# Kernel tuning notes

Measured on AMD Instinct MI355X. Metric: run time of the kernel, lower is better.

Reference implementation:

```python
import jax, jax.numpy as jnp
import numpy as np

N_NODE = 100_000
N_EDGE = 2_000_000
IN_DIM = 64
OUT_DIM = 64
ATTN_DIM = 32
N_REL = 200   # rela_embed has 2*N_REL+1 = 401 rows
N_ENT = 50_000
BATCH = 8


def setup_inputs() -> dict:
    key = jax.random.key(0)
    ks = jax.random.split(key, 16)
    # edges columns: 0=r_idx (query index in batch), 2=rel, 4=sub, 5=obj; cols 1,3 unused
    r_idx = jax.random.randint(ks[0], (N_EDGE,), 0, BATCH, dtype=jnp.int32)
    rel = jax.random.randint(ks[1], (N_EDGE,), 0, 2 * N_REL + 1, dtype=jnp.int32)
    sub = jax.random.randint(ks[2], (N_EDGE,), 0, N_NODE, dtype=jnp.int32)
    obj = jax.random.randint(ks[3], (N_EDGE,), 0, N_NODE, dtype=jnp.int32)
    pad = jnp.zeros((N_EDGE,), jnp.int32)
    edges = jnp.stack([r_idx, pad, rel, pad, sub, obj], axis=1)
    nodes = jnp.stack(
        [jax.random.randint(ks[4], (N_NODE,), 0, BATCH, dtype=jnp.int32),
         jax.random.randint(ks[5], (N_NODE,), 0, N_ENT, dtype=jnp.int32)], axis=1)
    s = 0.05
    return {
        "q_sub": jax.random.randint(ks[6], (BATCH,), 0, N_ENT, dtype=jnp.int32),
        "q_rel": jax.random.randint(ks[7], (BATCH,), 0, 2 * N_REL + 1, dtype=jnp.int32),
        "hidden": jax.random.normal(ks[8], (N_NODE, IN_DIM), jnp.float32),
        "edges": edges,
        "nodes": nodes,
        "old_nodes_new_idx": jnp.arange(N_NODE // 2, dtype=jnp.int32),
        "batchsize": BATCH,
        "rela_embed": jax.random.normal(ks[9], (2 * N_REL + 1, IN_DIM), jnp.float32) * s,
        "Ws": jax.random.normal(ks[10], (ATTN_DIM, IN_DIM), jnp.float32) * s,
        "Wr": jax.random.normal(ks[11], (ATTN_DIM, IN_DIM), jnp.float32) * s,
        "Wqr": jax.random.normal(ks[12], (ATTN_DIM, IN_DIM), jnp.float32) * s,
        "bqr": jax.random.normal(ks[13], (ATTN_DIM,), jnp.float32) * s,
        "w_alpha_w": jax.random.normal(ks[14], (1, ATTN_DIM), jnp.float32) * s,
        "w_alpha_b": jnp.zeros((1,), jnp.float32),
        "Wh": jax.random.normal(ks[15], (OUT_DIM, IN_DIM), jnp.float32) * s,
    }


def reference(q_sub, q_rel, hidden, edges, nodes, old_nodes_new_idx, batchsize,
              rela_embed, Ws, Wr, Wqr, bqr, w_alpha_w, w_alpha_b, Wh):
    sub = edges[:, 4]
    rel = edges[:, 2]
    obj = edges[:, 5]
    r_idx = edges[:, 0]
    n_node = hidden.shape[0]

    hs = hidden[sub]                      # [E, in_dim] gather
    hr = rela_embed[rel]                  # [E, in_dim] gather
    h_qr = rela_embed[q_rel][r_idx]       # [E, in_dim] gather of per-query rel embed

    # attention: sigmoid(w_alpha(relu(Ws hs + Wr hr + Wqr h_qr + bqr)))
    attn = jax.nn.relu(hs @ Ws.T + hr @ Wr.T + h_qr @ Wqr.T + bqr)  # [E, attn_dim]
    alpha = jax.nn.sigmoid(attn @ w_alpha_w.T + w_alpha_b)           # [E, 1]

    message = alpha * (hs + hr)           # [E, in_dim]
    message_agg = jax.ops.segment_sum(message, obj, num_segments=n_node)  # [n_node, in_dim]
    hidden_new = message_agg @ Wh.T       # act is identity (default)
    return hidden_new
```

## Files before the change

### kernel.cpp

```cpp
#include <hip/hip_runtime.h>
#include <hip/hip_bf16.h>
#include <hip/hip_fp16.h>


typedef __attribute__((ext_vector_type(8))) short bf16x8;
typedef __attribute__((ext_vector_type(4))) float f32x4;
typedef __attribute__((ext_vector_type(2))) float f32x2;

__device__ inline unsigned short f2bf(float x) {
    unsigned u = __float_as_uint(x);
    u += 0x7FFF + ((u >> 16) & 1);
    return (unsigned short)(u >> 16);
}
__device__ inline float bf2f(unsigned short b) {
    return __uint_as_float(((unsigned)b) << 16);
}
__device__ inline __half2 u2h2(unsigned u) {
    return __builtin_bit_cast(__half2, u);
}

__device__ inline bf16x8 pack8(float4 a, float4 b) {
    bf16x8 r;
    r[0] = (short)f2bf(a.x); r[1] = (short)f2bf(a.y);
    r[2] = (short)f2bf(a.z); r[3] = (short)f2bf(a.w);
    r[4] = (short)f2bf(b.x); r[5] = (short)f2bf(b.y);
    r[6] = (short)f2bf(b.z); r[7] = (short)f2bf(b.w);
    return r;
}

template<int NT, bool F16>
__global__ void proj_mfma2_kernel(const float* __restrict__ X1, int n1,
                                  const float* __restrict__ X2, int n2,
                                  const float* __restrict__ W,
                                  unsigned short* __restrict__ out1,
                                  unsigned short* __restrict__ out2) {
    int nb1 = (n1 + 63) / 64;
    const float* X; unsigned short* out; int nrows, mblk;
    if ((int)blockIdx.x < nb1) { X = X1; out = out1; nrows = n1; mblk = blockIdx.x; }
    else                        { X = X2; out = out2; nrows = n2; mblk = blockIdx.x - nb1; }

    int lane = threadIdx.x & 63;
    int wv   = threadIdx.x >> 6;
    int m0   = (mblk * 4 + wv) * 16;
    if (m0 >= nrows) return;
    int lr = lane & 15;
    int lk = lane >> 4;

    bf16x8 bfr[NT][2];
#pragma unroll
    for (int nt = 0; nt < NT; ++nt)
#pragma unroll
        for (int ks = 0; ks < 2; ++ks) {
            const float* wp = W + (size_t)(nt * 16 + lr) * 64 + ks * 32 + lk * 8;
            float4 w0 = *(const float4*)wp;
            float4 w1 = *(const float4*)(wp + 4);
            bfr[nt][ks] = pack8(w0, w1);
        }

    int row = m0 + lr;
    if (row >= nrows) row = nrows - 1;
    const float* xp = X + (size_t)row * 64 + lk * 8;
    float4 x0 = *(const float4*)xp;
    float4 x1 = *(const float4*)(xp + 4);
    float4 x2 = *(const float4*)(xp + 32);
    float4 x3 = *(const float4*)(xp + 36);
    bf16x8 a0 = pack8(x0, x1);
    bf16x8 a1 = pack8(x2, x3);

    f32x4 acc[NT];
#pragma unroll
    for (int nt = 0; nt < NT; ++nt) {
        acc[nt] = (f32x4){0.f, 0.f, 0.f, 0.f};
        acc[nt] = __builtin_amdgcn_mfma_f32_16x16x32_bf16(a0, bfr[nt][0], acc[nt], 0, 0, 0);
        acc[nt] = __builtin_amdgcn_mfma_f32_16x16x32_bf16(a1, bfr[nt][1], acc[nt], 0, 0, 0);
    }

#pragma unroll
    for (int nt = 0; nt < NT; ++nt)
#pragma unroll
        for (int r = 0; r < 4; ++r) {
            int ro = m0 + lk * 4 + r;
            if (ro < nrows) {
                unsigned short bits;
                if (F16) {
                    __half h = __float2half(acc[nt][r]);
                    bits = __builtin_bit_cast(unsigned short, h);
                } else {
                    bits = f2bf(acc[nt][r]);
                }
                out[(size_t)ro * (NT * 16) + nt * 16 + lr] = bits;
            }
        }
}

__global__ void qproj_bf16_kernel(const int* __restrict__ q_rel, const float* __restrict__ rela,
                                  const float* __restrict__ Wqr, const float* __restrict__ bqr,
                                  unsigned* __restrict__ Qb, int batch) {
    int tid = threadIdx.x;
    int b = tid >> 5, k = tid & 31;
    if (b >= batch) return;
    int qr = q_rel[b];
    const float* x = rela + (size_t)qr * 64;
    const float* w = Wqr + (size_t)k * 64;
    float acc = bqr[k];
    for (int d = 0; d < 64; ++d) acc += w[d] * x[d];
    float other = __shfl_xor(acc, 1, 64);
    if ((k & 1) == 0) {
        unsigned lo = f2bf(acc), hi = f2bf(other);
        Qb[b * 16 + (k >> 1)] = lo | (hi << 16);
    }
}

__global__ void pack_hist_kernel(const int4* __restrict__ edges4, int2* __restrict__ pk2,
                                 int* __restrict__ hmat, int n_edge, int NB) {
    __shared__ int hist[256];
    int tid = threadIdx.x, blk = blockIdx.x;
    hist[tid] = 0;
    __syncthreads();
    int unit0 = blk * 2048;
#pragma unroll
    for (int k = 0; k < 8; ++k) {
        int u = unit0 + k * 256 + tid;
        int base = u * 4;
        if (base >= n_edge) break;
        if (base + 4 <= n_edge) {
            const int4* p = edges4 + (size_t)u * 6;
            int4 v0 = p[0], v1 = p[1], v2 = p[2], v3 = p[3], v4 = p[4], v5 = p[5];
            atomicAdd(&hist[v1.y >> 9], 1);
            atomicAdd(&hist[v2.w >> 9], 1);
            atomicAdd(&hist[v4.y >> 9], 1);
            atomicAdd(&hist[v5.w >> 9], 1);
            int4 o0, o1;
            o0.x = v1.x | (v0.z << 17); o0.y = v1.y | (v0.x << 17);
            o0.z = v2.z | (v2.x << 17); o0.w = v2.w | (v1.z << 17);
            o1.x = v4.x | (v3.z << 17); o1.y = v4.y | (v3.x << 17);
            o1.z = v5.z | (v5.x << 17); o1.w = v5.w | (v4.z << 17);
            int4* q = (int4*)pk2 + (size_t)u * 2;
            q[0] = o0;
            q[1] = o1;
        } else {
            const int* ei = (const int*)edges4;
            for (int e = base; e < n_edge; ++e) {
                const int* ep = ei + (size_t)e * 6;
                int ridx = ep[0], rel = ep[2], sub = ep[4], obj = ep[5];
                atomicAdd(&hist[obj >> 9], 1);
                pk2[e] = make_int2(sub | (rel << 17), obj | (ridx << 17));
            }
        }
    }
    __syncthreads();
    hmat[tid * NB + blk] = hist[tid];
}

#define SCAN_CHUNK 1024

__global__ void scan_partial_kernel(const int* __restrict__ counts, int* __restrict__ bsum,
                                    int N) {
    __shared__ int s[256];
    int base = blockIdx.x * SCAN_CHUNK;
    int tid = threadIdx.x;
    int sum = 0;
#pragma unroll
    for (int k = 0; k < 4; ++k) {
        int idx = base + k * 256 + tid;
        if (idx < N) sum += counts[idx];
    }
    s[tid] = sum;
    __syncthreads();
    for (int off = 128; off > 0; off >>= 1) {
        if (tid < off) s[tid] += s[tid + off];
        __syncthreads();
    }
    if (tid == 0) bsum[blockIdx.x] = s[0];
}

__global__ void scan_bsum_kernel(int* __restrict__ bsum, int* __restrict__ offs, int B, int N) {
    __shared__ int s[1024];
    int tid = threadIdx.x;
    int v = (tid < B) ? bsum[tid] : 0;
    s[tid] = v;
    __syncthreads();
    for (int off = 1; off < 1024; off <<= 1) {
        int t = (tid >= off) ? s[tid - off] : 0;
        __syncthreads();
        s[tid] += t;
        __syncthreads();
    }
    if (tid < B) bsum[tid] = s[tid] - v;
    if (tid == 0) offs[N] = s[1023];
}

__global__ void scan_final_kernel(const int* __restrict__ counts, const int* __restrict__ bsum,
                                  int* __restrict__ offs, int N) {
    __shared__ int s[256];
    int base = blockIdx.x * SCAN_CHUNK;
    int tid = threadIdx.x;
    int v[4];
    int sum = 0;
#pragma unroll
    for (int k = 0; k < 4; ++k) {
        int idx = base + tid * 4 + k;
        v[k] = (idx < N) ? counts[idx] : 0;
        sum += v[k];
    }
    s[tid] = sum;
    __syncthreads();
    for (int off = 1; off < 256; off <<= 1) {
        int t = (tid >= off) ? s[tid - off] : 0;
        __syncthreads();
        s[tid] += t;
        __syncthreads();
    }
    int run = bsum[blockIdx.x] + s[tid] - sum;
#pragma unroll
    for (int k = 0; k < 4; ++k) {
        int idx = base + tid * 4 + k;
        if (idx < N) offs[idx] = run;
        run += v[k];
    }
}

__global__ void scatter1_kernel(const int2* __restrict__ pk2, const int* __restrict__ hscan,
                                int2* __restrict__ outrec, int n_edge, int NB) {
    __shared__ int cur[256];
    int tid = threadIdx.x, blk = blockIdx.x;
    cur[tid] = hscan[tid * NB + blk];
    __syncthreads();
    int unit0 = blk * 2048;
#pragma unroll
    for (int k = 0; k < 8; ++k) {
        int u = unit0 + k * 256 + tid;
        int base = u * 4;
        if (base >= n_edge) break;
        if (base + 4 <= n_edge) {
            const int4* q = (const int4*)pk2 + (size_t)u * 2;
            int4 a = q[0], b = q[1];
            int p0 = atomicAdd(&cur[(a.y >> 9) & 0xFF], 1);
            int p1 = atomicAdd(&cur[(a.w >> 9) & 0xFF], 1);
            int p2 = atomicAdd(&cur[(b.y >> 9) & 0xFF], 1);
            int p3 = atomicAdd(&cur[(b.w >> 9) & 0xFF], 1);
            outrec[p0] = make_int2(a.x, a.y);
            outrec[p1] = make_int2(a.z, a.w);
            outrec[p2] = make_int2(b.x, b.y);
            outrec[p3] = make_int2(b.z, b.w);
        } else {
            for (int e = base; e < n_edge; ++e) {
                int2 r = pk2[e];
                int p = atomicAdd(&cur[(r.y >> 9) & 0xFF], 1);
                outrec[p] = r;
            }
        }
    }
}

#define BS_CAP 12288
__global__ __launch_bounds__(512) void bucket_sort_kernel(const int2* __restrict__ in,
                                                          const int* __restrict__ hscan,
                                                          int2* __restrict__ out,
                                                          int* __restrict__ offs,
                                                          int NB, int n_node) {
    __shared__ int hist[512];
    __shared__ int sbase[512];
    __shared__ int cur[512];
    __shared__ int2 st[BS_CAP];
    int b = blockIdx.x, tid = threadIdx.x;
    int start = hscan[b * NB];
    int end   = hscan[(b + 1) * NB];
    int size  = end - start;
    hist[tid] = 0;
    __syncthreads();
    bool inlds = (size <= BS_CAP);
    if (inlds) {
        for (int i = tid; i < size; i += 512) {
            int2 v = in[start + i];
            st[i] = v;
            atomicAdd(&hist[v.y & 511], 1);
        }
    } else {
        for (int i = tid; i < size; i += 512) {
            int2 v = in[start + i];
            atomicAdd(&hist[v.y & 511], 1);
        }
    }
    __syncthreads();
    int h = hist[tid];
    sbase[tid] = h;
    __syncthreads();
    for (int off = 1; off < 512; off <<= 1) {
        int t = (tid >= off) ? sbase[tid - off] : 0;
        __syncthreads();
        sbase[tid] += t;
        __syncthreads();
    }
    int ebase = sbase[tid] - h;
    cur[tid] = ebase;
    int obj = (b << 9) | tid;
    if (obj <= n_node) offs[obj] = start + ebase;
    __syncthreads();
    if (inlds) {
        for (int i = tid; i < size; i += 512) {
            int2 r = st[i];
            int p = atomicAdd(&cur[r.y & 511], 1);
            out[start + p] = r;
        }
    } else {
        for (int i = tid; i < size; i += 512) {
            int2 r = in[start + i];
            int p = atomicAdd(&cur[r.y & 511], 1);
            out[start + p] = r;
        }
    }
}

__device__ inline float edot(unsigned sv, unsigned rv, unsigned qv, float2 w) {
    float a0 = fmaxf(bf2f((unsigned short)sv) + bf2f((unsigned short)rv)
                     + bf2f((unsigned short)qv), 0.f);
    float a1 = fmaxf(bf2f((unsigned short)(sv >> 16)) + bf2f((unsigned short)(rv >> 16))
                     + bf2f((unsigned short)(qv >> 16)), 0.f);
    return a0 * w.x + a1 * w.y;
}

__global__ void alpha_kernel(const int2* __restrict__ pk2,
                             const unsigned* __restrict__ Sb,
                             const unsigned* __restrict__ Rb,
                             const unsigned* __restrict__ Qb,
                             const float2* __restrict__ w2,
                             const float* __restrict__ w_alpha_b,
                             float2* __restrict__ rec,
                             int n_edge) {
    int tid = threadIdx.x;
    int lane = tid & 15;
    int e0 = (blockIdx.x * 16 + (tid >> 4)) * 4;
    if (e0 >= n_edge) return;
    int eN = n_edge - 1;
    int2 h0 = pk2[e0];
    int2 h1 = pk2[min(e0 + 1, eN)];
    int2 h2 = pk2[min(e0 + 2, eN)];
    int2 h3 = pk2[min(e0 + 3, eN)];
    float2 w = w2[lane];
    unsigned sv0 = Sb[(size_t)(h0.x & 0x1FFFF) * 16 + lane];
    unsigned sv1 = Sb[(size_t)(h1.x & 0x1FFFF) * 16 + lane];
    unsigned sv2 = Sb[(size_t)(h2.x & 0x1FFFF) * 16 + lane];
    unsigned sv3 = Sb[(size_t)(h3.x & 0x1FFFF) * 16 + lane];
    unsigned rv0 = Rb[(size_t)(h0.x >> 17) * 16 + lane];
    unsigned rv1 = Rb[(size_t)(h1.x >> 17) * 16 + lane];
    unsigned rv2 = Rb[(size_t)(h2.x >> 17) * 16 + lane];
    unsigned rv3 = Rb[(size_t)(h3.x >> 17) * 16 + lane];
    unsigned qv0 = Qb[((h0.y >> 17) & 7) * 16 + lane];
    unsigned qv1 = Qb[((h1.y >> 17) & 7) * 16 + lane];
    unsigned qv2 = Qb[((h2.y >> 17) & 7) * 16 + lane];
    unsigned qv3 = Qb[((h3.y >> 17) & 7) * 16 + lane];
    float p0 = edot(sv0, rv0, qv0, w);
    float p1 = edot(sv1, rv1, qv1, w);
    float p2 = edot(sv2, rv2, qv2, w);
    float p3 = edot(sv3, rv3, qv3, w);
#pragma unroll
    for (int off = 8; off > 0; off >>= 1) {
        p0 += __shfl_xor(p0, off, 16);
        p1 += __shfl_xor(p1, off, 16);
        p2 += __shfl_xor(p2, off, 16);
        p3 += __shfl_xor(p3, off, 16);
    }
    if (lane < 4 && e0 + lane < n_edge) {
        float p = p0; int2 h = h0;
        if (lane == 1) { p = p1; h = h1; }
        if (lane == 2) { p = p2; h = h2; }
        if (lane == 3) { p = p3; h = h3; }
        float alpha = 1.f / (1.f + __expf(-(p + w_alpha_b[0])));
        float2 out;
        out.x = alpha;
        out.y = __int_as_float(h.x);
        rec[e0 + lane] = out;
    }
}

__global__ void reduce_kernel(const float2* __restrict__ rec, const int* __restrict__ offs,
                              const uint2* __restrict__ Hw2,
                              const uint2* __restrict__ Rw2,
                              float4* __restrict__ out4, int n_node) {
    int lane = threadIdx.x & 63;
    int node = blockIdx.x * 4 + (threadIdx.x >> 6);
    if (node >= n_node) return;
    int g = lane >> 4;
    int t = lane & 15;
    int start = offs[node], end = offs[node + 1];
    __half2 acc0 = __float2half2_rn(0.f);
    __half2 acc1 = __float2half2_rn(0.f);

    for (int i = start; i < end; i += 64) {
        int m = end - i;
        if (m > 64) m = 64;
        float a = 0.f;
        int pk = 0;
        if (lane < m) {
            f32x2 r = __builtin_nontemporal_load((const f32x2*)&rec[i + lane]);
            a = r.x;
            pk = __float_as_int(r.y);
        }
        int nj = (m + 3) >> 2;

        __half2 A0, A1, A2, A3;
        uint2 H0, H1, H2, H3, R0, R1, R2, R3;

#define RD_ISSUE(S, J) do {                                                   \
        int src_ = 4 * (J) + g;                                               \
        bool ok_ = (src_ < m);                                                \
        int s_ = ok_ ? src_ : 0;                                              \
        float a_ = __shfl(a, s_, 64);                                         \
        int p_ = __shfl(pk, s_, 64);                                          \
        A##S = __float2half2_rn(ok_ ? a_ : 0.f);                              \
        int sub_ = p_ & 0x1FFFF, rel_ = p_ >> 17;                             \
        H##S = Hw2[(size_t)sub_ * 16 + t];                                    \
        R##S = Rw2[(size_t)rel_ * 16 + t];                                    \
    } while (0)

#define RD_CONSUME(S) do {                                                    \
        acc0 = __hfma2(A##S, __hadd2(u2h2(H##S.x), u2h2(R##S.x)), acc0);      \
        acc1 = __hfma2(A##S, __hadd2(u2h2(H##S.y), u2h2(R##S.y)), acc1);      \
    } while (0)

        RD_ISSUE(0, 0);
        RD_ISSUE(1, 1);
        RD_ISSUE(2, 2);
        RD_ISSUE(3, 3);
        for (int j = 0; j < nj; j += 4) {
            RD_CONSUME(0); RD_ISSUE(0, j + 4);
            RD_CONSUME(1); RD_ISSUE(1, j + 5);
            RD_CONSUME(2); RD_ISSUE(2, j + 6);
            RD_CONSUME(3); RD_ISSUE(3, j + 7);
        }
#undef RD_ISSUE
#undef RD_CONSUME
    }
    float2 f0 = __half22float2(acc0);
    float2 f1 = __half22float2(acc1);
    f32x4 acc = (f32x4){f0.x, f0.y, f1.x, f1.y};
#pragma unroll
    for (int off = 16; off <= 32; off <<= 1) {
        acc.x += __shfl_xor(acc.x, off, 64);
        acc.y += __shfl_xor(acc.y, off, 64);
        acc.z += __shfl_xor(acc.z, off, 64);
        acc.w += __shfl_xor(acc.w, off, 64);
    }
    if (g == 0)
        __builtin_nontemporal_store(acc, (f32x4*)&out4[(size_t)node * 16 + t]);
}

extern "C" void kernel_launch(void* const* d_in, const int* in_sizes, int n_in,
                              void* d_out, int out_size, void* d_ws, size_t ws_size,
                              hipStream_t stream) {
    const int*   q_rel     = (const int*)d_in[1];
    const float* hidden    = (const float*)d_in[2];
    const int*   edges     = (const int*)d_in[3];
    const float* rela      = (const float*)d_in[7];
    const float* Ws        = (const float*)d_in[8];
    const float* Wr        = (const float*)d_in[9];
    const float* Wqr       = (const float*)d_in[10];
    const float* bqr       = (const float*)d_in[11];
    const float* w_alpha_w = (const float*)d_in[12];
    const float* w_alpha_b = (const float*)d_in[13];
    const float* Wh        = (const float*)d_in[14];

    int n_node = in_sizes[2] / 64;
    int n_edge = in_sizes[3] / 6;
    int n_rel  = in_sizes[7] / 64;
    int batch  = in_sizes[1];

    int NB = (n_edge + 8191) / 8192;
    int N2 = NB * 256;
    int n_sblk2 = (N2 + SCAN_CHUNK - 1) / SCAN_CHUNK;

    unsigned* Sb   = (unsigned*)d_ws;
    unsigned* Rb   = Sb + (size_t)n_node * 16;
    unsigned* Qb   = Rb + (size_t)n_rel * 16;
    int*   offs    = (int*)(Qb + (size_t)batch * 16);
    int*   bsum    = offs + n_node + 1;
    int*   hmat    = bsum + 1024;
    int*   hscan   = hmat + N2;
    size_t rec_off = (size_t)(hscan + N2 + 1 - (int*)d_ws);
    rec_off = (rec_off + 3) & ~(size_t)3;
    float2* rec    = (float2*)((int*)d_ws + rec_off);
    int2*  pk2     = (int2*)(rec + n_edge);
    unsigned short* Hw = (unsigned short*)pk2;
    unsigned short* Rw = Hw + (size_t)n_node * 64;

    {
        int nb = (n_node + 63) / 64 + (n_rel + 63) / 64;
        proj_mfma2_kernel<2, false><<<nb, 256, 0, stream>>>(
            hidden, n_node, rela, n_rel, Ws, (unsigned short*)Sb, (unsigned short*)Rb);
    }
    qproj_bf16_kernel<<<1, 256, 0, stream>>>(q_rel, rela, Wqr, bqr, Qb, batch);

    pack_hist_kernel<<<NB, 256, 0, stream>>>((const int4*)edges, pk2, hmat, n_edge, NB);

    scan_partial_kernel<<<n_sblk2, 256, 0, stream>>>(hmat, bsum, N2);
    scan_bsum_kernel<<<1, 1024, 0, stream>>>(bsum, hscan, n_sblk2, N2);
    scan_final_kernel<<<n_sblk2, 256, 0, stream>>>(hmat, bsum, hscan, N2);

    scatter1_kernel<<<NB, 256, 0, stream>>>(pk2, hscan, (int2*)rec, n_edge, NB);
    bucket_sort_kernel<<<256, 512, 0, stream>>>((const int2*)rec, hscan, pk2, offs,
                                                NB, n_node);

    alpha_kernel<<<(n_edge + 63) / 64, 256, 0, stream>>>(
        pk2, Sb, Rb, Qb, (const float2*)w_alpha_w, w_alpha_b, rec, n_edge);

    {
        int nb = (n_node + 63) / 64 + (n_rel + 63) / 64;
        proj_mfma2_kernel<4, true><<<nb, 256, 0, stream>>>(
            hidden, n_node, rela, n_rel, Wh, Hw, Rw);
    }

    reduce_kernel<<<(n_node + 3) / 4, 256, 0, stream>>>(
        rec, offs, (const uint2*)Hw, (const uint2*)Rw, (float4*)d_out, n_node);
}
```

Measured before the change: 308.4 us.

## Process multiple nodes per wave in reduce kernel with prefetch of next node's records

```diff
diff --git a/kernel.cpp b/kernel.cpp
--- a/kernel.cpp
+++ b/kernel.cpp
@@ -377,30 +377,58 @@
 __global__ void reduce_kernel(const float2* __restrict__ rec, const int* __restrict__ offs,
                               const uint2* __restrict__ Hw2,
                               const uint2* __restrict__ Rw2,
-                              float4* __restrict__ out4, int n_node) {
+                              float4* __restrict__ out4, int n_node, int K) {
     int lane = threadIdx.x & 63;
-    int node = blockIdx.x * 4 + (threadIdx.x >> 6);
-    if (node >= n_node) return;
+    int wid = blockIdx.x * (blockDim.x >> 6) + (threadIdx.x >> 6);
     int g = lane >> 4;
     int t = lane & 15;
-    int start = offs[node], end = offs[node + 1];
-    __half2 acc0 = __float2half2_rn(0.f);
-    __half2 acc1 = __float2half2_rn(0.f);
-
-    for (int i = start; i < end; i += 64) {
-        int m = end - i;
-        if (m > 64) m = 64;
-        float a = 0.f;
-        int pk = 0;
+    int n0 = wid * K;
+    if (n0 >= n_node) return;
+    int nmax = n_node - n0;
+    if (nmax > K) nmax = K;
+    int offl = (lane <= nmax) ? offs[n0 + lane] : 0;
+
+    float aC = 0.f; int pkC = 0;
+    {
+        int s = __shfl(offl, 0, 64), e = __shfl(offl, 1, 64);
+        int m = e - s; if (m > 64) m = 64;
         if (lane < m) {
-            f32x2 r = __builtin_nontemporal_load((const f32x2*)&rec[i + lane]);
-            a = r.x;
-            pk = __float_as_int(r.y);
-        }
-        int nj = (m + 3) >> 2;
-
-        __half2 A0, A1, A2, A3;
-        uint2 H0, H1, H2, H3, R0, R1, R2, R3;
+            f32x2 r = __builtin_nontemporal_load((const f32x2*)&rec[s + lane]);
+            aC = r.x; pkC = __float_as_int(r.y);
+        }
+    }
+
+    for (int i = 0; i < nmax; ++i) {
+        int s = __shfl(offl, i, 64);
+        int e = __shfl(offl, i + 1, 64);
+        float aN = 0.f; int pkN = 0;
+        if (i + 1 < nmax) {
+            int en = __shfl(offl, i + 2, 64);
+            int mn = en - e; if (mn > 64) mn = 64;
+            if (lane < mn) {
+                f32x2 r = __builtin_nontemporal_load((const f32x2*)&rec[e + lane]);
+                aN = r.x; pkN = __float_as_int(r.y);
+            }
+        }
+
+        __half2 acc0 = __float2half2_rn(0.f);
+        __half2 acc1 = __float2half2_rn(0.f);
+
+        for (int b = s; b < e; b += 64) {
+            int m = e - b; if (m > 64) m = 64;
+            float a; int pk;
+            if (b == s) { a = aC; pk = pkC; }
+            else {
+                a = 0.f; pk = 0;
+                if (lane < m) {
+                    f32x2 r = __builtin_nontemporal_load((const f32x2*)&rec[b + lane]);
+                    a = r.x; pk = __float_as_int(r.y);
+                }
+            }
+            int nj = (m + 3) >> 2;
+
+            __half2 A0, A1, A2, A3;
+            uint2 H0, H1, H2, H3, R0, R1, R2, R3;
 
 #define RD_ISSUE(S, J) do {                                                   \
         int src_ = 4 * (J) + g;                                               \
@@ -419,31 +447,34 @@
         acc1 = __hfma2(A##S, __hadd2(u2h2(H##S.y), u2h2(R##S.y)), acc1);      \
     } while (0)
 
-        RD_ISSUE(0, 0);
-        RD_ISSUE(1, 1);
-        RD_ISSUE(2, 2);
-        RD_ISSUE(3, 3);
-        for (int j = 0; j < nj; j += 4) {
-            RD_CONSUME(0); RD_ISSUE(0, j + 4);
-            RD_CONSUME(1); RD_ISSUE(1, j + 5);
-            RD_CONSUME(2); RD_ISSUE(2, j + 6);
-            RD_CONSUME(3); RD_ISSUE(3, j + 7);
-        }
+            RD_ISSUE(0, 0);
+            RD_ISSUE(1, 1);
+            RD_ISSUE(2, 2);
+            RD_ISSUE(3, 3);
+            for (int j = 0; j < nj; j += 4) {
+                RD_CONSUME(0); RD_ISSUE(0, j + 4);
+                RD_CONSUME(1); RD_ISSUE(1, j + 5);
+                RD_CONSUME(2); RD_ISSUE(2, j + 6);
+                RD_CONSUME(3); RD_ISSUE(3, j + 7);
+            }
 #undef RD_ISSUE
 #undef RD_CONSUME
-    }
-    float2 f0 = __half22float2(acc0);
-    float2 f1 = __half22float2(acc1);
-    f32x4 acc = (f32x4){f0.x, f0.y, f1.x, f1.y};
-#pragma unroll
-    for (int off = 16; off <= 32; off <<= 1) {
-        acc.x += __shfl_xor(acc.x, off, 64);
-        acc.y += __shfl_xor(acc.y, off, 64);
-        acc.z += __shfl_xor(acc.z, off, 64);
-        acc.w += __shfl_xor(acc.w, off, 64);
-    }
-    if (g == 0)
-        __builtin_nontemporal_store(acc, (f32x4*)&out4[(size_t)node * 16 + t]);
+        }
+
+        float2 f0 = __half22float2(acc0);
+        float2 f1 = __half22float2(acc1);
+        f32x4 acc = (f32x4){f0.x, f0.y, f1.x, f1.y};
+#pragma unroll
+        for (int off = 16; off <= 32; off <<= 1) {
+            acc.x += __shfl_xor(acc.x, off, 64);
+            acc.y += __shfl_xor(acc.y, off, 64);
+            acc.z += __shfl_xor(acc.z, off, 64);
+            acc.w += __shfl_xor(acc.w, off, 64);
+        }
+        if (g == 0)
+            __builtin_nontemporal_store(acc, (f32x4*)&out4[(size_t)(n0 + i) * 16 + t]);
+        aC = aN; pkC = pkN;
+    }
 }
 
 extern "C" void kernel_launch(void* const* d_in, const int* in_sizes, int n_in,
@@ -510,6 +541,11 @@
             hidden, n_node, rela, n_rel, Wh, Hw, Rw);
     }
 
-    reduce_kernel<<<(n_node + 3) / 4, 256, 0, stream>>>(
-        rec, offs, (const uint2*)Hw, (const uint2*)Rw, (float4*)d_out, n_node);
-}
+    {
+        int nwaves = 8192;
+        int K = (n_node + nwaves - 1) / nwaves;
+        int nblk = (n_node + K * 4 - 1) / (K * 4);
+        reduce_kernel<<<nblk, 256, 0, stream>>>(
+            rec, offs, (const uint2*)Hw, (const uint2*)Rw, (float4*)d_out, n_node, K);
+    }
+}
```

Result: slower. 318.7 us (+3.3%).

## Fuse bucket sort scatter with alpha computation into one kernel

Applied to the files above, without the earlier changes.

```diff
diff --git a/kernel.cpp b/kernel.cpp
--- a/kernel.cpp
+++ b/kernel.cpp
@@ -253,65 +253,6 @@
     }
 }
 
-#define BS_CAP 12288
-__global__ __launch_bounds__(512) void bucket_sort_kernel(const int2* __restrict__ in,
-                                                          const int* __restrict__ hscan,
-                                                          int2* __restrict__ out,
-                                                          int* __restrict__ offs,
-                                                          int NB, int n_node) {
-    __shared__ int hist[512];
-    __shared__ int sbase[512];
-    __shared__ int cur[512];
-    __shared__ int2 st[BS_CAP];
-    int b = blockIdx.x, tid = threadIdx.x;
-    int start = hscan[b * NB];
-    int end   = hscan[(b + 1) * NB];
-    int size  = end - start;
-    hist[tid] = 0;
-    __syncthreads();
-    bool inlds = (size <= BS_CAP);
-    if (inlds) {
-        for (int i = tid; i < size; i += 512) {
-            int2 v = in[start + i];
-            st[i] = v;
-            atomicAdd(&hist[v.y & 511], 1);
-        }
-    } else {
-        for (int i = tid; i < size; i += 512) {
-            int2 v = in[start + i];
-            atomicAdd(&hist[v.y & 511], 1);
-        }
-    }
-    __syncthreads();
-    int h = hist[tid];
-    sbase[tid] = h;
-    __syncthreads();
-    for (int off = 1; off < 512; off <<= 1) {
-        int t = (tid >= off) ? sbase[tid - off] : 0;
-        __syncthreads();
-        sbase[tid] += t;
-        __syncthreads();
-    }
-    int ebase = sbase[tid] - h;
-    cur[tid] = ebase;
-    int obj = (b << 9) | tid;
-    if (obj <= n_node) offs[obj] = start + ebase;
-    __syncthreads();
-    if (inlds) {
-        for (int i = tid; i < size; i += 512) {
-            int2 r = st[i];
-            int p = atomicAdd(&cur[r.y & 511], 1);
-            out[start + p] = r;
-        }
-    } else {
-        for (int i = tid; i < size; i += 512) {
-            int2 r = in[start + i];
-            int p = atomicAdd(&cur[r.y & 511], 1);
-            out[start + p] = r;
-        }
-    }
-}
-
 __device__ inline float edot(unsigned sv, unsigned rv, unsigned qv, float2 w) {
     float a0 = fmaxf(bf2f((unsigned short)sv) + bf2f((unsigned short)rv)
                      + bf2f((unsigned short)qv), 0.f);
@@ -320,57 +261,84 @@
     return a0 * w.x + a1 * w.y;
 }
 
-__global__ void alpha_kernel(const int2* __restrict__ pk2,
-                             const unsigned* __restrict__ Sb,
-                             const unsigned* __restrict__ Rb,
-                             const unsigned* __restrict__ Qb,
-                             const float2* __restrict__ w2,
-                             const float* __restrict__ w_alpha_b,
-                             float2* __restrict__ rec,
-                             int n_edge) {
-    int tid = threadIdx.x;
+__global__ __launch_bounds__(512) void bucket_alpha_kernel(
+        const int2* __restrict__ in, const int* __restrict__ hscan,
+        const unsigned* __restrict__ Sb, const unsigned* __restrict__ Rb,
+        const unsigned* __restrict__ Qb, const float2* __restrict__ w2,
+        const float* __restrict__ w_alpha_b, float2* __restrict__ rec,
+        int* __restrict__ offs, int NB, int n_node) {
+    __shared__ int hist[512];
+    __shared__ int sbase[512];
+    __shared__ int cur[512];
+    int b = blockIdx.x, tid = threadIdx.x;
+    int start = hscan[b * NB];
+    int end   = hscan[(b + 1) * NB];
+    int size  = end - start;
+    hist[tid] = 0;
+    __syncthreads();
+    for (int i = tid; i < size; i += 512)
+        atomicAdd(&hist[in[start + i].y & 511], 1);
+    __syncthreads();
+    int h = hist[tid];
+    sbase[tid] = h;
+    __syncthreads();
+    for (int off = 1; off < 512; off <<= 1) {
+        int t = (tid >= off) ? sbase[tid - off] : 0;
+        __syncthreads();
+        sbase[tid] += t;
+        __syncthreads();
+    }
+    int ebase = sbase[tid] - h;
+    cur[tid] = ebase;
+    int obj = (b << 9) | tid;
+    if (obj <= n_node) offs[obj] = start + ebase;
+    __syncthreads();
+
+    if (size == 0) return;
     int lane = tid & 15;
-    int e0 = (blockIdx.x * 16 + (tid >> 4)) * 4;
-    if (e0 >= n_edge) return;
-    int eN = n_edge - 1;
-    int2 h0 = pk2[e0];
-    int2 h1 = pk2[min(e0 + 1, eN)];
-    int2 h2 = pk2[min(e0 + 2, eN)];
-    int2 h3 = pk2[min(e0 + 3, eN)];
     float2 w = w2[lane];
-    unsigned sv0 = Sb[(size_t)(h0.x & 0x1FFFF) * 16 + lane];
-    unsigned sv1 = Sb[(size_t)(h1.x & 0x1FFFF) * 16 + lane];
-    unsigned sv2 = Sb[(size_t)(h2.x & 0x1FFFF) * 16 + lane];
-    unsigned sv3 = Sb[(size_t)(h3.x & 0x1FFFF) * 16 + lane];
-    unsigned rv0 = Rb[(size_t)(h0.x >> 17) * 16 + lane];
-    unsigned rv1 = Rb[(size_t)(h1.x >> 17) * 16 + lane];
-    unsigned rv2 = Rb[(size_t)(h2.x >> 17) * 16 + lane];
-    unsigned rv3 = Rb[(size_t)(h3.x >> 17) * 16 + lane];
-    unsigned qv0 = Qb[((h0.y >> 17) & 7) * 16 + lane];
-    unsigned qv1 = Qb[((h1.y >> 17) & 7) * 16 + lane];
-    unsigned qv2 = Qb[((h2.y >> 17) & 7) * 16 + lane];
-    unsigned qv3 = Qb[((h3.y >> 17) & 7) * 16 + lane];
-    float p0 = edot(sv0, rv0, qv0, w);
-    float p1 = edot(sv1, rv1, qv1, w);
-    float p2 = edot(sv2, rv2, qv2, w);
-    float p3 = edot(sv3, rv3, qv3, w);
-#pragma unroll
-    for (int off = 8; off > 0; off >>= 1) {
-        p0 += __shfl_xor(p0, off, 16);
-        p1 += __shfl_xor(p1, off, 16);
-        p2 += __shfl_xor(p2, off, 16);
-        p3 += __shfl_xor(p3, off, 16);
-    }
-    if (lane < 4 && e0 + lane < n_edge) {
-        float p = p0; int2 h = h0;
-        if (lane == 1) { p = p1; h = h1; }
-        if (lane == 2) { p = p2; h = h2; }
-        if (lane == 3) { p = p3; h = h3; }
-        float alpha = 1.f / (1.f + __expf(-(p + w_alpha_b[0])));
-        float2 out;
-        out.x = alpha;
-        out.y = __int_as_float(h.x);
-        rec[e0 + lane] = out;
+    float wb = w_alpha_b[0];
+    int last = size - 1;
+    for (int e0 = (tid >> 4) * 4; e0 < size; e0 += 128) {
+        int2 h0 = in[start + min(e0 + 0, last)];
+        int2 h1 = in[start + min(e0 + 1, last)];
+        int2 h2 = in[start + min(e0 + 2, last)];
+        int2 h3 = in[start + min(e0 + 3, last)];
+        unsigned sv0 = Sb[(size_t)(h0.x & 0x1FFFF) * 16 + lane];
+        unsigned sv1 = Sb[(size_t)(h1.x & 0x1FFFF) * 16 + lane];
+        unsigned sv2 = Sb[(size_t)(h2.x & 0x1FFFF) * 16 + lane];
+        unsigned sv3 = Sb[(size_t)(h3.x & 0x1FFFF) * 16 + lane];
+        unsigned rv0 = Rb[(size_t)(h0.x >> 17) * 16 + lane];
+        unsigned rv1 = Rb[(size_t)(h1.x >> 17) * 16 + lane];
+        unsigned rv2 = Rb[(size_t)(h2.x >> 17) * 16 + lane];
+        unsigned rv3 = Rb[(size_t)(h3.x >> 17) * 16 + lane];
+        unsigned qv0 = Qb[((h0.y >> 17) & 7) * 16 + lane];
+        unsigned qv1 = Qb[((h1.y >> 17) & 7) * 16 + lane];
+        unsigned qv2 = Qb[((h2.y >> 17) & 7) * 16 + lane];
+        unsigned qv3 = Qb[((h3.y >> 17) & 7) * 16 + lane];
+        float p0 = edot(sv0, rv0, qv0, w);
+        float p1 = edot(sv1, rv1, qv1, w);
+        float p2 = edot(sv2, rv2, qv2, w);
+        float p3 = edot(sv3, rv3, qv3, w);
+#pragma unroll
+        for (int off = 8; off > 0; off >>= 1) {
+            p0 += __shfl_xor(p0, off, 16);
+            p1 += __shfl_xor(p1, off, 16);
+            p2 += __shfl_xor(p2, off, 16);
+            p3 += __shfl_xor(p3, off, 16);
+        }
+        if (lane < 4 && e0 + lane < size) {
+            float p = p0; int2 hh = h0;
+            if (lane == 1) { p = p1; hh = h1; }
+            if (lane == 2) { p = p2; hh = h2; }
+            if (lane == 3) { p = p3; hh = h3; }
+            float alpha = 1.f / (1.f + __expf(-(p + wb)));
+            int pos = atomicAdd(&cur[hh.y & 511], 1);
+            float2 o;
+            o.x = alpha;
+            o.y = __int_as_float(hh.x);
+            rec[start + pos] = o;
+        }
     }
 }
 
@@ -479,9 +447,10 @@
     int*   hscan   = hmat + N2;
     size_t rec_off = (size_t)(hscan + N2 + 1 - (int*)d_ws);
     rec_off = (rec_off + 3) & ~(size_t)3;
-    float2* rec    = (float2*)((int*)d_ws + rec_off);
-    int2*  pk2     = (int2*)(rec + n_edge);
-    unsigned short* Hw = (unsigned short*)pk2;
+    int2*  regA    = (int2*)((int*)d_ws + rec_off);
+    int2*  regB    = regA + n_edge;
+    float2* rec    = (float2*)regB;
+    unsigned short* Hw = (unsigned short*)regA;
     unsigned short* Rw = Hw + (size_t)n_node * 64;
 
     {
@@ -491,18 +460,17 @@
     }
     qproj_bf16_kernel<<<1, 256, 0, stream>>>(q_rel, rela, Wqr, bqr, Qb, batch);
 
-    pack_hist_kernel<<<NB, 256, 0, stream>>>((const int4*)edges, pk2, hmat, n_edge, NB);
+    pack_hist_kernel<<<NB, 256, 0, stream>>>((const int4*)edges, regB, hmat, n_edge, NB);
 
     scan_partial_kernel<<<n_sblk2, 256, 0, stream>>>(hmat, bsum, N2);
     scan_bsum_kernel<<<1, 1024, 0, stream>>>(bsum, hscan, n_sblk2, N2);
     scan_final_kernel<<<n_sblk2, 256, 0, stream>>>(hmat, bsum, hscan, N2);
 
-    scatter1_kernel<<<NB, 256, 0, stream>>>(pk2, hscan, (int2*)rec, n_edge, NB);
-    bucket_sort_kernel<<<256, 512, 0, stream>>>((const int2*)rec, hscan, pk2, offs,
-                                                NB, n_node);
-
-    alpha_kernel<<<(n_edge + 63) / 64, 256, 0, stream>>>(
-        pk2, Sb, Rb, Qb, (const float2*)w_alpha_w, w_alpha_b, rec, n_edge);
+    scatter1_kernel<<<NB, 256, 0, stream>>>(regB, hscan, regA, n_edge, NB);
+
+    bucket_alpha_kernel<<<256, 512, 0, stream>>>(
+        regA, hscan, Sb, Rb, Qb, (const float2*)w_alpha_w, w_alpha_b,
+        rec, offs, NB, n_node);
 
     {
         int nb = (n_node + 63) / 64 + (n_rel + 63) / 64;
```

Measured after the change: 352.5 us. 1.14x slower.
